# Optimization experiments

Measured on AMD Instinct MI355X. Metric: run time of the kernel, lower is better.

## Reference

```python
import jax, jax.numpy as jnp
import numpy as np

NMIX = 10  # mixtures in discretized mix of logistics


def _causal_mask(kh, kw, include_center):
    # rows strictly above center fully visible; center row left of center; optionally center
    m = np.zeros((kh, kw), dtype=np.float32)
    m[: kh // 2, :] = 1.0
    m[kh // 2, : kw // 2] = 1.0
    if include_center:
        m[kh // 2, kw // 2] = 1.0
    return jnp.asarray(m)[None, None]  # [1,1,kh,kw] broadcast over O,I


def _conv(x, w):
    return jax.lax.conv_general_dilated(
        x, w, (1, 1), 'SAME', dimension_numbers=('NCHW', 'OIHW', 'NCHW'))


def pixelcnn_params(x, w_in, w_blk, w_out1, w_out2):
    mA = _causal_mask(7, 7, False)
    mB = _causal_mask(3, 3, True)
    h = _conv(x, w_in * mA)                      # [B,160,H,W]
    for i in range(w_blk.shape[0]):              # 5 gated resnet blocks
        g = _conv(jax.nn.relu(h), w_blk[i] * mB)  # [B,320,H,W]
        a, b = jnp.split(g, 2, axis=1)
        h = h + jnp.tanh(a) * jax.nn.sigmoid(b)
    h = jax.nn.relu(_conv(jax.nn.relu(h), w_out1))
    return _conv(h, w_out2)                      # [B,100,H,W]


def dmol_log_prob(x, params):
    # x: [B,3,H,W] in [-1,1]; params: [B,100,H,W]; returns per-example log prob [B]
    B, C, H, W = x.shape
    l = jnp.transpose(params, (0, 2, 3, 1))       # [B,H,W,100]
    xt = jnp.transpose(x, (0, 2, 3, 1))           # [B,H,W,3]
    logit_probs = l[..., :NMIX]                   # [B,H,W,10]
    rest = l[..., NMIX:].reshape(B, H, W, 3, 3 * NMIX)
    means = rest[..., :NMIX]
    log_scales = jnp.maximum(rest[..., NMIX:2 * NMIX], -7.0)
    coeffs = jnp.tanh(rest[..., 2 * NMIX:])
    xe = xt[..., None]                            # [B,H,W,3,1]
    m1 = means[..., 0, :]
    m2 = means[..., 1, :] + coeffs[..., 0, :] * xe[..., 0, :]
    m3 = means[..., 2, :] + coeffs[..., 1, :] * xe[..., 0, :] + coeffs[..., 2, :] * xe[..., 1, :]
    means_adj = jnp.stack([m1, m2, m3], axis=3)   # [B,H,W,3,10]
    centered = xe - means_adj
    inv_stdv = jnp.exp(-log_scales)
    plus_in = inv_stdv * (centered + 1.0 / 255.0)
    min_in = inv_stdv * (centered - 1.0 / 255.0)
    cdf_delta = jax.nn.sigmoid(plus_in) - jax.nn.sigmoid(min_in)
    log_cdf_plus = plus_in - jax.nn.softplus(plus_in)
    log_one_minus_cdf_min = -jax.nn.softplus(min_in)
    mid_in = inv_stdv * centered
    log_pdf_mid = mid_in - log_scales - 2.0 * jax.nn.softplus(mid_in)
    log_prob_in = jnp.where(cdf_delta > 1e-5,
                            jnp.log(jnp.clip(cdf_delta, 1e-12, None)),
                            log_pdf_mid - np.float32(np.log(127.5)))
    log_probs_c = jnp.where(xe < -0.999, log_cdf_plus,
                            jnp.where(xe > 0.999, log_one_minus_cdf_min, log_prob_in))
    log_probs = jnp.sum(log_probs_c, axis=3) + jax.nn.log_softmax(logit_probs, axis=-1)
    lp = jax.scipy.special.logsumexp(log_probs, axis=-1)  # [B,H,W]
    return jnp.sum(lp, axis=(1, 2))                       # [B]


def setup_inputs() -> dict:
    key = jax.random.key(0)
    ks = jax.random.split(key, 5)
    F = 160
    return {
        'samples': jax.random.uniform(ks[0], (16, 3, 64, 64), dtype=jnp.float32),
        'w_in': jax.random.normal(ks[1], (F, 3, 7, 7), dtype=jnp.float32) * 0.05,
        'w_blk': jax.random.normal(ks[2], (5, 2 * F, F, 3, 3), dtype=jnp.float32) * 0.03,
        'w_out1': jax.random.normal(ks[3], (F, F, 1, 1), dtype=jnp.float32) * 0.05,
        'w_out2': jax.random.normal(ks[4], (100, F, 1, 1), dtype=jnp.float32) * 0.05,
    }


def reference(samples, w_in, w_blk, w_out1, w_out2):
    x = samples * 2.0 - 1.0
    params = pixelcnn_params(x, w_in, w_blk, w_out1, w_out2)
    return dmol_log_prob(x, params)
```

## Files before the change

kernel.cpp:

```cpp
#include <hip/hip_runtime.h>
#include <math.h>


using short8  = __attribute__((ext_vector_type(8))) short;
using short4v = __attribute__((ext_vector_type(4))) short;
using f32x4   = __attribute__((ext_vector_type(4))) float;

static constexpr float L2E = 1.44269504088896f;
static constexpr float LN2 = 0.69314718055995f;

__device__ __forceinline__ float fexp2(float x) { return __builtin_amdgcn_exp2f(x); }
__device__ __forceinline__ float flog2(float x) { return __builtin_amdgcn_logf(x); }
__device__ __forceinline__ float frcp(float x)  { return __builtin_amdgcn_rcpf(x); }
__device__ __forceinline__ float fexp(float x)  { return fexp2(x * L2E); }
__device__ __forceinline__ float flog(float x)  { return flog2(x) * LN2; }
__device__ __forceinline__ float fsigmoid(float x) { return frcp(1.f + fexp2(-x * L2E)); }
__device__ __forceinline__ float ftanh(float x)    { return 1.f - 2.f * frcp(1.f + fexp2(x * (2.f * L2E))); }
__device__ __forceinline__ float fsoftplus(float z) {
    float e = fexp2(-fabsf(z) * L2E);
    return fmaxf(z, 0.f) + flog2(1.f + e) * LN2;
}

__device__ __forceinline__ unsigned pk_bf16(float a, float b) {
    union { float f; unsigned u; } ua, ub; ua.f = a; ub.f = b;
    return __builtin_amdgcn_perm(ub.u + 0x7fffu, ua.u + 0x7fffu, 0x07060302u);
}

__device__ __forceinline__ short f2bf(float f) {
    union { float f; unsigned u; } v; v.f = f;
    unsigned r = (v.u + 0x7fffu + ((v.u >> 16) & 1u)) >> 16;
    return (short)r;
}

__device__ __forceinline__ float bf2f(unsigned short s) {
    union { unsigned u; float f; } v; v.u = ((unsigned)s) << 16; return v.f;
}

__device__ __forceinline__ unsigned relu2(unsigned v) {
    unsigned m = ((v & 0x80008000u) >> 15) * 0xffffu;
    return v & ~m;
}

static constexpr size_t X_OFF    = 0;
static constexpr size_t WINP_OFF = 786432;
static constexpr size_t W1P_OFF  = 817152;
static constexpr size_t W2P_OFF  = 868352;
static constexpr size_t WPB_OFF  = 919552;
static constexpr size_t HA_OFF   = 3479552;
static constexpr size_t HB_OFF   = 24451072;

__global__ void k_prep(const float* __restrict__ s, float* __restrict__ x, int n) {
    int i = blockIdx.x * 256 + threadIdx.x;
    if (i < n) x[i] = 2.f * s[i] - 1.f;
}

__global__ void k_twb(const float* __restrict__ w, short* __restrict__ wP) {
    int idx = blockIdx.x * 256 + threadIdx.x;
    if (idx >= 5 * 25 * 320 * 32) return;
    int icl = idx & 31;
    int oc  = (idx >> 5) % 320;
    int kt  = ((idx >> 5) / 320) % 25;
    int i   = idx / (25 * 320 * 32);
    int tap = kt / 5, ic = (kt % 5) * 32 + icl;
    const int ky[5] = {0,0,0,1,1}, kx[5] = {0,1,2,0,1};
    float v = w[(((size_t)(i * 320 + oc) * 160 + ic) * 3 + ky[tap]) * 3 + kx[tap]];
    wP[idx] = f2bf(v);
}

__global__ void k_twin(const float* __restrict__ w, short* __restrict__ wP) {
    int idx = blockIdx.x * 256 + threadIdx.x;
    if (idx >= 3 * 160 * 32) return;
    int icl = idx & 31;
    int oc  = (idx >> 5) % 160;
    int kc  = idx / 5120;
    int k = kc * 32 + icl;
    short v = 0;
    if (k < 72) {
        int tap = k / 3, ic = k % 3;
        int ky = (tap < 21) ? tap / 7 : 3;
        int kx = (tap < 21) ? tap % 7 : tap - 21;
        v = f2bf(w[((oc * 3 + ic) * 7 + ky) * 7 + kx]);
    }
    wP[idx] = v;
}

__global__ void k_tw1(const float* __restrict__ w, short* __restrict__ wP) {
    int idx = blockIdx.x * 256 + threadIdx.x;
    if (idx >= 5 * 160 * 32) return;
    int icl = idx & 31;
    int oc  = (idx >> 5) % 160;
    int kc  = idx / 5120;
    wP[idx] = f2bf(w[oc * 160 + kc * 32 + icl]);
}

__global__ void k_tw2(const float* __restrict__ w, short* __restrict__ wP) {
    int idx = blockIdx.x * 256 + threadIdx.x;
    if (idx >= 5 * 160 * 32) return;
    int icl = idx & 31;
    int oc  = (idx >> 5) % 160;
    int kc  = idx / 5120;
    wP[idx] = (oc < 100) ? f2bf(w[oc * 160 + kc * 32 + icl]) : (short)0;
}

__global__ __launch_bounds__(320) void k_convin(const float* __restrict__ X,
                                                const short* __restrict__ WINP,
                                                unsigned short* __restrict__ hout) {
    __shared__ float xls[3 * 4 * 40];
    __shared__ short Bls[32 * 104];
    int y = blockIdx.x >> 1, half = blockIdx.x & 1, b = blockIdx.y;
    int xbase = half * 32;
    int t = threadIdx.x;
    for (int i = t; i < 456; i += 320) {
        int col = i % 38; int r = (i / 38) % 4; int ic = i / 152;
        int xg = xbase + col - 3, yg = y + r - 3;
        float v = 0.f;
        if (xg >= 0 && xg < 64 && yg >= 0)
            v = X[((size_t)(b * 3 + ic) * 64 + yg) * 64 + xg];
        xls[(ic * 4 + r) * 40 + col] = v;
    }
    __syncthreads();
    for (int i = t; i < 3072; i += 320) {
        int k = i % 96; int px = i / 96;
        short v = 0;
        if (k < 72) {
            int tap = k / 3, ic = k % 3;
            int ky = (tap < 21) ? tap / 7 : 3;
            int kx = (tap < 21) ? tap % 7 : tap - 21;
            v = f2bf(xls[(ic * 4 + ky) * 40 + px + kx]);
        }
        Bls[px * 104 + k] = v;
    }
    __syncthreads();
    int lane = t & 63, w = t >> 6;
    int lx = lane & 15, q = lane >> 4;
    f32x4 acc[2][2] = {};
    const short* wl = WINP + lx * 32 + q * 8;
    #pragma unroll
    for (int kc = 0; kc < 3; ++kc) {
        short8 aF[2], bF[2];
        aF[0] = *(const short8*)(wl + (kc * 160 + 32 * w) * 32);
        aF[1] = *(const short8*)(wl + (kc * 160 + 32 * w + 16) * 32);
        #pragma unroll
        for (int nt = 0; nt < 2; ++nt)
            bF[nt] = *(const short8*)&Bls[(nt * 16 + lx) * 104 + kc * 32 + q * 8];
        #pragma unroll
        for (int mt = 0; mt < 2; ++mt)
            #pragma unroll
            for (int nt = 0; nt < 2; ++nt)
                acc[mt][nt] = __builtin_amdgcn_mfma_f32_16x16x32_bf16(
                    aF[mt], bF[nt], acc[mt][nt], 0, 0, 0);
    }
    size_t rowbase = ((size_t)(b * 64 + y)) * 64 * 160;
    #pragma unroll
    for (int mt = 0; mt < 2; ++mt) {
        int c0 = 32 * w + mt * 16 + q * 4;
        #pragma unroll
        for (int nt = 0; nt < 2; ++nt) {
            int px = xbase + nt * 16 + lx;
            uint2 o;
            o.x = pk_bf16(acc[mt][nt][0], acc[mt][nt][1]);
            o.y = pk_bf16(acc[mt][nt][2], acc[mt][nt][3]);
            *(uint2*)&hout[rowbase + (size_t)px * 160 + c0] = o;
        }
    }
}

__global__ __launch_bounds__(320, 2) void k_blk(const unsigned short* __restrict__ hin,
                                                unsigned short* __restrict__ hout,
                                                const short* __restrict__ wP) {
    __shared__ short in_s[3 * 66 * 160];
    int y0 = blockIdx.x * 2, b = blockIdx.y;
    int t = threadIdx.x;
    for (int i = t; i < 3960; i += 320) {
        int c8 = i % 20; int xl = (i / 20) % 66; int r = i / 1320;
        int xg = xl - 1, yg = y0 + r - 1;
        uint4 v = {0u, 0u, 0u, 0u};
        if (xg >= 0 && xg < 64 && yg >= 0) {
            v = *(const uint4*)&hin[(((size_t)(b * 64 + yg)) * 64 + xg) * 160 + c8 * 8];
            v.x = relu2(v.x); v.y = relu2(v.y); v.z = relu2(v.z); v.w = relu2(v.w);
        }
        *(uint4*)&in_s[(r * 66 + xl) * 160 + c8 * 8] = v;
    }
    __syncthreads();

    int lane = t & 63, w = t >> 6;
    int lx = lane & 15, q = lane >> 4;
    f32x4 acc[4][8] = {};
    const short* wl = wP + lx * 32 + q * 8;
    const int dxs[5] = {-1, 0, 1, -1, 0};
    const int rws[5] = {0, 0, 0, 1, 1};
    #pragma unroll
    for (int tap = 0; tap < 5; ++tap) {
        #pragma unroll
        for (int k5 = 0; k5 < 5; ++k5) {
            const short* wk = wl + (tap * 5 + k5) * 10240;
            short8 aF[4];
            aF[0] = *(const short8*)(wk + (32 * w) * 32);
            aF[1] = *(const short8*)(wk + (32 * w + 16) * 32);
            aF[2] = *(const short8*)(wk + (160 + 32 * w) * 32);
            aF[3] = *(const short8*)(wk + (176 + 32 * w) * 32);
            #pragma unroll
            for (int nt = 0; nt < 8; ++nt) {
                int rr = rws[tap] + (nt >> 2);
                int xc = 1 + dxs[tap] + (nt & 3) * 16 + lx;
                short8 bF = *(const short8*)&in_s[(rr * 66 + xc) * 160 + k5 * 32 + q * 8];
                #pragma unroll
                for (int mt = 0; mt < 4; ++mt)
                    acc[mt][nt] = __builtin_amdgcn_mfma_f32_16x16x32_bf16(
                        aF[mt], bF, acc[mt][nt], 0, 0, 0);
            }
        }
    }
    #pragma unroll
    for (int mt = 0; mt < 2; ++mt) {
        int c0 = 32 * w + mt * 16 + q * 4;
        #pragma unroll
        for (int nt = 0; nt < 8; ++nt) {
            int y = y0 + (nt >> 2);
            int px = (nt & 3) * 16 + lx;
            size_t off = (((size_t)(b * 64 + y)) * 64 + px) * 160 + c0;
            ushort4 hv = *(const ushort4*)&hin[off];
            float o0 = bf2f(hv.x) + ftanh(acc[mt][nt][0]) * fsigmoid(acc[mt + 2][nt][0]);
            float o1 = bf2f(hv.y) + ftanh(acc[mt][nt][1]) * fsigmoid(acc[mt + 2][nt][1]);
            float o2 = bf2f(hv.z) + ftanh(acc[mt][nt][2]) * fsigmoid(acc[mt + 2][nt][2]);
            float o3 = bf2f(hv.w) + ftanh(acc[mt][nt][3]) * fsigmoid(acc[mt + 2][nt][3]);
            uint2 o;
            o.x = pk_bf16(o0, o1);
            o.y = pk_bf16(o2, o3);
            *(uint2*)&hout[off] = o;
        }
    }
}

__global__ __launch_bounds__(320) void k_head(const unsigned short* __restrict__ hin,
                                              const short* __restrict__ W1P,
                                              const short* __restrict__ W2P,
                                              const float* __restrict__ X,
                                              float* __restrict__ out) {
    __shared__ char arena[14848];
    __shared__ short h2ls[32 * 168];
    short* hls = (short*)arena;
    float* Pls = (float*)arena;
    float* lpls = (float*)(arena + 13312);
    int y = blockIdx.x >> 1, half = blockIdx.x & 1, b = blockIdx.y;
    int xbase = half * 32;
    int t = threadIdx.x;
    size_t rowbase = ((size_t)(b * 64 + y)) * 64 * 160;
    for (int i = t; i < 640; i += 320) {
        int c8 = i % 20; int px = i / 20;
        uint4 v = *(const uint4*)&hin[rowbase + (size_t)(xbase + px) * 160 + c8 * 8];
        v.x = relu2(v.x); v.y = relu2(v.y); v.z = relu2(v.z); v.w = relu2(v.w);
        *(uint4*)&hls[px * 168 + c8 * 8] = v;
    }
    __syncthreads();
    int lane = t & 63, w = t >> 6;
    int lx = lane & 15, q = lane >> 4;
    {
        f32x4 acc[2][2] = {};
        const short* wl = W1P + lx * 32 + q * 8;
        #pragma unroll
        for (int kc = 0; kc < 5; ++kc) {
            short8 aF[2], bF[2];
            aF[0] = *(const short8*)(wl + (kc * 160 + 32 * w) * 32);
            aF[1] = *(const short8*)(wl + (kc * 160 + 32 * w + 16) * 32);
            #pragma unroll
            for (int nt = 0; nt < 2; ++nt)
                bF[nt] = *(const short8*)&hls[(nt * 16 + lx) * 168 + kc * 32 + q * 8];
            #pragma unroll
            for (int mt = 0; mt < 2; ++mt)
                #pragma unroll
                for (int nt = 0; nt < 2; ++nt)
                    acc[mt][nt] = __builtin_amdgcn_mfma_f32_16x16x32_bf16(
                        aF[mt], bF[nt], acc[mt][nt], 0, 0, 0);
        }
        __syncthreads();
        #pragma unroll
        for (int mt = 0; mt < 2; ++mt) {
            int c0 = 32 * w + mt * 16 + q * 4;
            #pragma unroll
            for (int nt = 0; nt < 2; ++nt) {
                int px = nt * 16 + lx;
                union { short4v s; unsigned u[2]; } sv;
                sv.u[0] = pk_bf16(fmaxf(acc[mt][nt][0], 0.f), fmaxf(acc[mt][nt][1], 0.f));
                sv.u[1] = pk_bf16(fmaxf(acc[mt][nt][2], 0.f), fmaxf(acc[mt][nt][3], 0.f));
                *(short4v*)&h2ls[px * 168 + c0] = sv.s;
            }
        }
    }
    __syncthreads();
    {
        f32x4 acc[2][2] = {};
        const short* wl = W2P + lx * 32 + q * 8;
        #pragma unroll
        for (int kc = 0; kc < 5; ++kc) {
            short8 aF[2], bF[2];
            aF[0] = *(const short8*)(wl + (kc * 160 + 32 * w) * 32);
            aF[1] = *(const short8*)(wl + (kc * 160 + 32 * w + 16) * 32);
            #pragma unroll
            for (int nt = 0; nt < 2; ++nt)
                bF[nt] = *(const short8*)&h2ls[(nt * 16 + lx) * 168 + kc * 32 + q * 8];
            #pragma unroll
            for (int mt = 0; mt < 2; ++mt)
                #pragma unroll
                for (int nt = 0; nt < 2; ++nt)
                    acc[mt][nt] = __builtin_amdgcn_mfma_f32_16x16x32_bf16(
                        aF[mt], bF[nt], acc[mt][nt], 0, 0, 0);
        }
        #pragma unroll
        for (int mt = 0; mt < 2; ++mt) {
            int c0 = 32 * w + mt * 16 + q * 4;
            if (c0 < 100) {
                #pragma unroll
                for (int nt = 0; nt < 2; ++nt) {
                    int px = nt * 16 + lx;
                    float4 o;
                    o.x = acc[mt][nt][0]; o.y = acc[mt][nt][1];
                    o.z = acc[mt][nt][2]; o.w = acc[mt][nt][3];
                    *(float4*)&Pls[px * 104 + c0] = o;
                }
            }
        }
    }
    __syncthreads();
    const float LOG127P5 = 4.8481163504f;
    {
        int px = t & 31, m = t >> 5;
        const float* pp = &Pls[px * 104];
        float xs[3];
        #pragma unroll
        for (int c = 0; c < 3; ++c)
            xs[c] = X[((size_t)(b * 3 + c)) * 4096 + (size_t)y * 64 + xbase + px];
        float mx = pp[0];
        #pragma unroll
        for (int j = 1; j < 10; ++j) mx = fmaxf(mx, pp[j]);
        float se = 0.f;
        #pragma unroll
        for (int j = 0; j < 10; ++j) se += fexp(pp[j] - mx);
        float lse = mx + flog(se);
        float sum = pp[m] - lse;
        float mean0 = pp[10 + m];
        float mean1 = pp[40 + m];
        float mean2 = pp[70 + m];
        float ls0 = fmaxf(pp[20 + m], -7.f);
        float ls1 = fmaxf(pp[50 + m], -7.f);
        float ls2 = fmaxf(pp[80 + m], -7.f);
        float c0 = ftanh(pp[30 + m]);
        float c1 = ftanh(pp[60 + m]);
        float c2 = ftanh(pp[90 + m]);
        float mu[3], lsv[3];
        mu[0] = mean0;
        mu[1] = mean1 + c0 * xs[0];
        mu[2] = mean2 + c1 * xs[0] + c2 * xs[1];
        lsv[0] = ls0; lsv[1] = ls1; lsv[2] = ls2;
        #pragma unroll
        for (int ci = 0; ci < 3; ++ci) {
            float cent = xs[ci] - mu[ci];
            float inv = fexp(-lsv[ci]);
            float plus_in = inv * (cent + 1.f / 255.f);
            float min_in = inv * (cent - 1.f / 255.f);
            float cdf_delta = fsigmoid(plus_in) - fsigmoid(min_in);
            float log_cdf_plus = plus_in - fsoftplus(plus_in);
            float log_om_cdf = -fsoftplus(min_in);
            float mid = inv * cent;
            float log_pdf_mid = mid - lsv[ci] - 2.f * fsoftplus(mid);
            float lpi = (cdf_delta > 1e-5f) ? flog(fmaxf(cdf_delta, 1e-12f))
                                            : (log_pdf_mid - LOG127P5);
            float lpc = (xs[ci] < -0.999f) ? log_cdf_plus
                       : ((xs[ci] > 0.999f) ? log_om_cdf : lpi);
            sum += lpc;
        }
        lpls[px * 12 + m] = sum;
    }
    __syncthreads();
    if (t < 32) {
        int px = t;
        float mx2 = lpls[px * 12];
        #pragma unroll
        for (int m = 1; m < 10; ++m) mx2 = fmaxf(mx2, lpls[px * 12 + m]);
        float se2 = 0.f;
        #pragma unroll
        for (int m = 0; m < 10; ++m) se2 += fexp(lpls[px * 12 + m] - mx2);
        float lp = mx2 + flog(se2);
        lp += __shfl_down(lp, 16, 32);
        lp += __shfl_down(lp, 8, 32);
        lp += __shfl_down(lp, 4, 32);
        lp += __shfl_down(lp, 2, 32);
        lp += __shfl_down(lp, 1, 32);
        if (t == 0) atomicAdd(&out[b], lp);
    }
}

extern "C" void kernel_launch(void* const* d_in, const int* in_sizes, int n_in,
                              void* d_out, int out_size, void* d_ws, size_t ws_size,
                              hipStream_t stream) {
    const float* samples = (const float*)d_in[0];
    const float* w_in    = (const float*)d_in[1];
    const float* w_blk   = (const float*)d_in[2];
    const float* w_out1  = (const float*)d_in[3];
    const float* w_out2  = (const float*)d_in[4];
    char* ws = (char*)d_ws;
    float* X    = (float*)(ws + X_OFF);
    short* WINP = (short*)(ws + WINP_OFF);
    short* W1P  = (short*)(ws + W1P_OFF);
    short* W2P  = (short*)(ws + W2P_OFF);
    short* WPB  = (short*)(ws + WPB_OFF);
    unsigned short* HA = (unsigned short*)(ws + HA_OFF);
    unsigned short* HB = (unsigned short*)(ws + HB_OFF);
    float* fout = (float*)d_out;

    k_prep<<<768, 256, 0, stream>>>(samples, X, 16 * 3 * 4096);
    k_twb<<<5000, 256, 0, stream>>>(w_blk, WPB);
    k_twin<<<60, 256, 0, stream>>>(w_in, WINP);
    k_tw1<<<100, 256, 0, stream>>>(w_out1, W1P);
    k_tw2<<<100, 256, 0, stream>>>(w_out2, W2P);

    k_convin<<<dim3(128, 16), 320, 0, stream>>>(X, WINP, HA);

    unsigned short* a = HA; unsigned short* bq = HB;
    for (int i = 0; i < 5; i++) {
        k_blk<<<dim3(32, 16), 320, 0, stream>>>(a, bq, WPB + (size_t)i * 25 * 320 * 32);
        unsigned short* tmp = a; a = bq; bq = tmp;
    }
    hipMemsetAsync(d_out, 0, (size_t)out_size * sizeof(float), stream);
    k_head<<<dim3(128, 16), 320, 0, stream>>>(a, W1P, W2P, X, fout);
}
```

Measured before the change: 464.7 us.

## Store padded ReLU activation copy and use 32x32 MFMA with async LDS loads in block convs

Each producer kernel now also writes a ReLU-applied bf16 copy of h into a spatially padded buffer with zeroed halos, so the gated blocks can bulk-copy their input rows into LDS with global_load_lds and no bounds checks or per-element ReLU. The block kernel moves from 16x16x32 to 32x32x16 MFMA with a repacked weight layout. It also processes one output row per workgroup with twice as many workgroups and a higher occupancy target. This adds an extra activation write per layer and more redundant halo-row loads in exchange for simpler, faster staging and larger MFMA tiles.

```diff
diff --git a/kernel.cpp b/kernel.cpp
--- a/kernel.cpp
+++ b/kernel.cpp
@@ -5,9 +5,14 @@
 using short8  = __attribute__((ext_vector_type(8))) short;
 using short4v = __attribute__((ext_vector_type(4))) short;
 using f32x4   = __attribute__((ext_vector_type(4))) float;
+using f32x16  = __attribute__((ext_vector_type(16))) float;
 
 static constexpr float L2E = 1.44269504088896f;
 static constexpr float LN2 = 0.69314718055995f;
+
+static constexpr int CPAD = 168;
+static constexpr int RST  = 66 * CPAD;
+static constexpr int IST  = 65 * RST;
 
 __device__ __forceinline__ float fexp2(float x) { return __builtin_amdgcn_exp2f(x); }
 __device__ __forceinline__ float flog2(float x) { return __builtin_amdgcn_logf(x); }
@@ -36,11 +41,6 @@
     union { unsigned u; float f; } v; v.u = ((unsigned)s) << 16; return v.f;
 }
 
-__device__ __forceinline__ unsigned relu2(unsigned v) {
-    unsigned m = ((v & 0x80008000u) >> 15) * 0xffffu;
-    return v & ~m;
-}
-
 static constexpr size_t X_OFF    = 0;
 static constexpr size_t WINP_OFF = 786432;
 static constexpr size_t W1P_OFF  = 817152;
@@ -48,6 +48,8 @@
 static constexpr size_t WPB_OFF  = 919552;
 static constexpr size_t HA_OFF   = 3479552;
 static constexpr size_t HB_OFF   = 24451072;
+static constexpr size_t HRA_OFF  = 45422592;
+static constexpr size_t HRB_OFF  = 68485632;
 
 __global__ void k_prep(const float* __restrict__ s, float* __restrict__ x, int n) {
     int i = blockIdx.x * 256 + threadIdx.x;
@@ -56,12 +58,16 @@
 
 __global__ void k_twb(const float* __restrict__ w, short* __restrict__ wP) {
     int idx = blockIdx.x * 256 + threadIdx.x;
-    if (idx >= 5 * 25 * 320 * 32) return;
-    int icl = idx & 31;
-    int oc  = (idx >> 5) % 320;
-    int kt  = ((idx >> 5) / 320) % 25;
-    int i   = idx / (25 * 320 * 32);
-    int tap = kt / 5, ic = (kt % 5) * 32 + icl;
+    if (idx >= 5 * 100 * 320 * 8) return;
+    int j  = idx & 7;
+    int r  = idx >> 3;
+    int oc = r % 320;
+    int r2 = r / 320;
+    int sp = r2 % 100;
+    int i  = r2 / 100;
+    int s = sp >> 1, pair = sp & 1;
+    int k = s * 16 + pair * 8 + j;
+    int tap = k / 160, ic = k - tap * 160;
     const int ky[5] = {0,0,0,1,1}, kx[5] = {0,1,2,0,1};
     float v = w[(((size_t)(i * 320 + oc) * 160 + ic) * 3 + ky[tap]) * 3 + kx[tap]];
     wP[idx] = f2bf(v);
@@ -102,9 +108,23 @@
     wP[idx] = (oc < 100) ? f2bf(w[oc * 160 + kc * 32 + icl]) : (short)0;
 }
 
+__global__ void k_halo(unsigned short* __restrict__ hrA, unsigned short* __restrict__ hrB) {
+    int i = blockIdx.x * 256 + threadIdx.x;
+    if (i >= 16 * 194 * CPAD) return;
+    int c = i % CPAD;
+    int r = (i / CPAD) % 194;
+    int b = i / (CPAD * 194);
+    int yp, xp;
+    if (r < 66) { yp = 0; xp = r; }
+    else { int rr = r - 66; yp = 1 + (rr >> 1); xp = (rr & 1) ? 65 : 0; }
+    unsigned short* p = blockIdx.y ? hrB : hrA;
+    p[((size_t)b * 65 + yp) * RST + (size_t)xp * CPAD + c] = 0;
+}
+
 __global__ __launch_bounds__(320) void k_convin(const float* __restrict__ X,
                                                 const short* __restrict__ WINP,
-                                                unsigned short* __restrict__ hout) {
+                                                unsigned short* __restrict__ hout,
+                                                unsigned short* __restrict__ hrout) {
     __shared__ float xls[3 * 4 * 40];
     __shared__ short Bls[32 * 104];
     int y = blockIdx.x >> 1, half = blockIdx.x & 1, b = blockIdx.y;
@@ -151,88 +171,97 @@
                     aF[mt], bF[nt], acc[mt][nt], 0, 0, 0);
     }
     size_t rowbase = ((size_t)(b * 64 + y)) * 64 * 160;
+    size_t rbase   = ((size_t)b * 65 + (y + 1)) * RST;
     #pragma unroll
     for (int mt = 0; mt < 2; ++mt) {
         int c0 = 32 * w + mt * 16 + q * 4;
         #pragma unroll
         for (int nt = 0; nt < 2; ++nt) {
             int px = xbase + nt * 16 + lx;
-            uint2 o;
-            o.x = pk_bf16(acc[mt][nt][0], acc[mt][nt][1]);
-            o.y = pk_bf16(acc[mt][nt][2], acc[mt][nt][3]);
-            *(uint2*)&hout[rowbase + (size_t)px * 160 + c0] = o;
-        }
-    }
-}
-
-__global__ __launch_bounds__(320, 2) void k_blk(const unsigned short* __restrict__ hin,
-                                                unsigned short* __restrict__ hout,
+            float o0 = acc[mt][nt][0], o1 = acc[mt][nt][1];
+            float o2 = acc[mt][nt][2], o3 = acc[mt][nt][3];
+            uint2 oh;
+            oh.x = pk_bf16(o0, o1); oh.y = pk_bf16(o2, o3);
+            *(uint2*)&hout[rowbase + (size_t)px * 160 + c0] = oh;
+            uint2 orr;
+            orr.x = pk_bf16(fmaxf(o0, 0.f), fmaxf(o1, 0.f));
+            orr.y = pk_bf16(fmaxf(o2, 0.f), fmaxf(o3, 0.f));
+            *(uint2*)&hrout[rbase + (size_t)(px + 1) * CPAD + c0] = orr;
+        }
+    }
+}
+
+__global__ __launch_bounds__(320, 4) void k_blk(const unsigned short* __restrict__ h_in,
+                                                unsigned short* __restrict__ h_out,
+                                                const unsigned short* __restrict__ hr_in,
+                                                unsigned short* __restrict__ hr_out,
                                                 const short* __restrict__ wP) {
-    __shared__ short in_s[3 * 66 * 160];
-    int y0 = blockIdx.x * 2, b = blockIdx.y;
+    __shared__ short in_s[2 * RST];
+    int y = blockIdx.x, b = blockIdx.y;
     int t = threadIdx.x;
-    for (int i = t; i < 3960; i += 320) {
-        int c8 = i % 20; int xl = (i / 20) % 66; int r = i / 1320;
-        int xg = xl - 1, yg = y0 + r - 1;
-        uint4 v = {0u, 0u, 0u, 0u};
-        if (xg >= 0 && xg < 64 && yg >= 0) {
-            v = *(const uint4*)&hin[(((size_t)(b * 64 + yg)) * 64 + xg) * 160 + c8 * 8];
-            v.x = relu2(v.x); v.y = relu2(v.y); v.z = relu2(v.z); v.w = relu2(v.w);
-        }
-        *(uint4*)&in_s[(r * 66 + xl) * 160 + c8 * 8] = v;
-    }
-    __syncthreads();
-
     int lane = t & 63, w = t >> 6;
-    int lx = lane & 15, q = lane >> 4;
-    f32x4 acc[4][8] = {};
-    const short* wl = wP + lx * 32 + q * 8;
+    {
+        const unsigned short* src = hr_in + ((size_t)b * 65 + y) * RST;
+        #pragma unroll
+        for (int r = 0; r < 9; ++r) {
+            int cb = __builtin_amdgcn_readfirstlane(r * 320 + w * 64);
+            if (cb + lane < 2772) {
+                __builtin_amdgcn_global_load_lds(
+                    (const __attribute__((address_space(1))) unsigned int*)(src + (size_t)(cb + lane) * 8),
+                    (__attribute__((address_space(3))) unsigned int*)(in_s + cb * 8),
+                    16, 0, 0);
+            }
+        }
+    }
+    __syncthreads();
+
+    int lm = lane & 31, pair = lane >> 5;
+    f32x16 acc[2][2] = {};
+    const short* waP = wP + pair * 2560 + (32 * w + lm) * 8;
     const int dxs[5] = {-1, 0, 1, -1, 0};
     const int rws[5] = {0, 0, 0, 1, 1};
     #pragma unroll
     for (int tap = 0; tap < 5; ++tap) {
-        #pragma unroll
-        for (int k5 = 0; k5 < 5; ++k5) {
-            const short* wk = wl + (tap * 5 + k5) * 10240;
-            short8 aF[4];
-            aF[0] = *(const short8*)(wk + (32 * w) * 32);
-            aF[1] = *(const short8*)(wk + (32 * w + 16) * 32);
-            aF[2] = *(const short8*)(wk + (160 + 32 * w) * 32);
-            aF[3] = *(const short8*)(wk + (176 + 32 * w) * 32);
-            #pragma unroll
-            for (int nt = 0; nt < 8; ++nt) {
-                int rr = rws[tap] + (nt >> 2);
-                int xc = 1 + dxs[tap] + (nt & 3) * 16 + lx;
-                short8 bF = *(const short8*)&in_s[(rr * 66 + xc) * 160 + k5 * 32 + q * 8];
-                #pragma unroll
-                for (int mt = 0; mt < 4; ++mt)
-                    acc[mt][nt] = __builtin_amdgcn_mfma_f32_16x16x32_bf16(
-                        aF[mt], bF, acc[mt][nt], 0, 0, 0);
-            }
-        }
-    }
+        int rb0 = (rws[tap] * 66 + 1 + dxs[tap] + lm) * CPAD + pair * 8;
+        #pragma unroll
+        for (int si = 0; si < 10; ++si) {
+            int s = tap * 10 + si;
+            short8 aA = *(const short8*)(waP + (size_t)s * 5120);
+            short8 aG = *(const short8*)(waP + 1280 + (size_t)s * 5120);
+            short8 b0 = *(const short8*)&in_s[rb0 + si * 16];
+            short8 b1 = *(const short8*)&in_s[rb0 + 32 * CPAD + si * 16];
+            acc[0][0] = __builtin_amdgcn_mfma_f32_32x32x16_bf16(aA, b0, acc[0][0], 0, 0, 0);
+            acc[0][1] = __builtin_amdgcn_mfma_f32_32x32x16_bf16(aA, b1, acc[0][1], 0, 0, 0);
+            acc[1][0] = __builtin_amdgcn_mfma_f32_32x32x16_bf16(aG, b0, acc[1][0], 0, 0, 0);
+            acc[1][1] = __builtin_amdgcn_mfma_f32_32x32x16_bf16(aG, b1, acc[1][1], 0, 0, 0);
+        }
+    }
+    size_t rowbase = ((size_t)(b * 64 + y)) * 64 * 160;
+    size_t rbase   = ((size_t)b * 65 + (y + 1)) * RST;
     #pragma unroll
-    for (int mt = 0; mt < 2; ++mt) {
-        int c0 = 32 * w + mt * 16 + q * 4;
-        #pragma unroll
-        for (int nt = 0; nt < 8; ++nt) {
-            int y = y0 + (nt >> 2);
-            int px = (nt & 3) * 16 + lx;
-            size_t off = (((size_t)(b * 64 + y)) * 64 + px) * 160 + c0;
-            ushort4 hv = *(const ushort4*)&hin[off];
-            float o0 = bf2f(hv.x) + ftanh(acc[mt][nt][0]) * fsigmoid(acc[mt + 2][nt][0]);
-            float o1 = bf2f(hv.y) + ftanh(acc[mt][nt][1]) * fsigmoid(acc[mt + 2][nt][1]);
-            float o2 = bf2f(hv.z) + ftanh(acc[mt][nt][2]) * fsigmoid(acc[mt + 2][nt][2]);
-            float o3 = bf2f(hv.w) + ftanh(acc[mt][nt][3]) * fsigmoid(acc[mt + 2][nt][3]);
-            uint2 o;
-            o.x = pk_bf16(o0, o1);
-            o.y = pk_bf16(o2, o3);
-            *(uint2*)&hout[off] = o;
-        }
-    }
-}
-
-__global__ __launch_bounds__(320) void k_head(const unsigned short* __restrict__ hin,
+    for (int n = 0; n < 2; ++n) {
+        int px = n * 32 + lm;
+        #pragma unroll
+        for (int qd = 0; qd < 4; ++qd) {
+            int c0 = 32 * w + qd * 8 + 4 * pair;
+            size_t offh = rowbase + (size_t)px * 160 + c0;
+            ushort4 hv = *(const ushort4*)&h_in[offh];
+            float o0 = bf2f(hv.x) + ftanh(acc[0][n][qd * 4 + 0]) * fsigmoid(acc[1][n][qd * 4 + 0]);
+            float o1 = bf2f(hv.y) + ftanh(acc[0][n][qd * 4 + 1]) * fsigmoid(acc[1][n][qd * 4 + 1]);
+            float o2 = bf2f(hv.z) + ftanh(acc[0][n][qd * 4 + 2]) * fsigmoid(acc[1][n][qd * 4 + 2]);
+            float o3 = bf2f(hv.w) + ftanh(acc[0][n][qd * 4 + 3]) * fsigmoid(acc[1][n][qd * 4 + 3]);
+            uint2 oh;
+            oh.x = pk_bf16(o0, o1); oh.y = pk_bf16(o2, o3);
+            *(uint2*)&h_out[offh] = oh;
+            uint2 orr;
+            orr.x = pk_bf16(fmaxf(o0, 0.f), fmaxf(o1, 0.f));
+            orr.y = pk_bf16(fmaxf(o2, 0.f), fmaxf(o3, 0.f));
+            *(uint2*)&hr_out[rbase + (size_t)(px + 1) * CPAD + c0] = orr;
+        }
+    }
+}
+
+__global__ __launch_bounds__(320) void k_head(const unsigned short* __restrict__ hr,
                                               const short* __restrict__ W1P,
                                               const short* __restrict__ W2P,
                                               const float* __restrict__ X,
@@ -245,11 +274,10 @@
     int y = blockIdx.x >> 1, half = blockIdx.x & 1, b = blockIdx.y;
     int xbase = half * 32;
     int t = threadIdx.x;
-    size_t rowbase = ((size_t)(b * 64 + y)) * 64 * 160;
+    size_t rbase = ((size_t)b * 65 + (y + 1)) * RST;
     for (int i = t; i < 640; i += 320) {
         int c8 = i % 20; int px = i / 20;
-        uint4 v = *(const uint4*)&hin[rowbase + (size_t)(xbase + px) * 160 + c8 * 8];
-        v.x = relu2(v.x); v.y = relu2(v.y); v.z = relu2(v.z); v.w = relu2(v.w);
+        uint4 v = *(const uint4*)&hr[rbase + (size_t)(xbase + px + 1) * CPAD + c8 * 8];
         *(uint4*)&hls[px * 168 + c8 * 8] = v;
     }
     __syncthreads();
@@ -404,8 +432,10 @@
     short* W1P  = (short*)(ws + W1P_OFF);
     short* W2P  = (short*)(ws + W2P_OFF);
     short* WPB  = (short*)(ws + WPB_OFF);
-    unsigned short* HA = (unsigned short*)(ws + HA_OFF);
-    unsigned short* HB = (unsigned short*)(ws + HB_OFF);
+    unsigned short* HA  = (unsigned short*)(ws + HA_OFF);
+    unsigned short* HB  = (unsigned short*)(ws + HB_OFF);
+    unsigned short* HRA = (unsigned short*)(ws + HRA_OFF);
+    unsigned short* HRB = (unsigned short*)(ws + HRB_OFF);
     float* fout = (float*)d_out;
 
     k_prep<<<768, 256, 0, stream>>>(samples, X, 16 * 3 * 4096);
@@ -413,14 +443,17 @@
     k_twin<<<60, 256, 0, stream>>>(w_in, WINP);
     k_tw1<<<100, 256, 0, stream>>>(w_out1, W1P);
     k_tw2<<<100, 256, 0, stream>>>(w_out2, W2P);
-
-    k_convin<<<dim3(128, 16), 320, 0, stream>>>(X, WINP, HA);
-
-    unsigned short* a = HA; unsigned short* bq = HB;
+    k_halo<<<dim3((16 * 194 * CPAD + 255) / 256, 2), 256, 0, stream>>>(HRA, HRB);
+
+    k_convin<<<dim3(128, 16), 320, 0, stream>>>(X, WINP, HA, HRA);
+
+    unsigned short* a = HA;  unsigned short* bq = HB;
+    unsigned short* ra = HRA; unsigned short* rb = HRB;
     for (int i = 0; i < 5; i++) {
-        k_blk<<<dim3(32, 16), 320, 0, stream>>>(a, bq, WPB + (size_t)i * 25 * 320 * 32);
+        k_blk<<<dim3(64, 16), 320, 0, stream>>>(a, bq, ra, rb, WPB + (size_t)i * 256000);
         unsigned short* tmp = a; a = bq; bq = tmp;
+        unsigned short* tr = ra; ra = rb; rb = tr;
     }
     hipMemsetAsync(d_out, 0, (size_t)out_size * sizeof(float), stream);
-    k_head<<<dim3(128, 16), 320, 0, stream>>>(a, W1P, W2P, X, fout);
-}
+    k_head<<<dim3(128, 16), 320, 0, stream>>>(ra, W1P, W2P, X, fout);
+}
```

Result: no change. 461.1 us (-0.8%).
